# Performance work log

Measured on AMD Instinct MI355X. Metric: run time of the kernel, lower is better.

Reference implementation:

```python
import jax, jax.numpy as jnp
import numpy as np

NUM_EXPERTS = 256
TOP_K = 8
HIDDEN = 7168
N_GROUP = 8
TOPK_GROUP = 4
ROUTED_SCALING_FACTOR = 2.5
NORM_TOPK_PROB = True
TOKENS = 8192


def setup_inputs() -> dict:
    key = jax.random.key(0)
    k1, k2, k3 = jax.random.split(key, 3)
    hidden_states = jax.random.normal(k1, (TOKENS, HIDDEN), dtype=jnp.float32)
    # small init scale keeps router logits in a reasonable sigmoid range
    weight = jax.random.normal(k2, (NUM_EXPERTS, HIDDEN), dtype=jnp.float32) * 0.02
    e_score_correction_bias = jax.random.normal(k3, (NUM_EXPERTS,), dtype=jnp.float32) * 0.01
    return {
        "hidden_states": hidden_states,
        "weight": weight,
        "e_score_correction_bias": e_score_correction_bias,
    }


def reference(hidden_states, weight, e_score_correction_bias):
    hs = hidden_states.reshape(-1, hidden_states.shape[-1]).astype(jnp.float32)
    # [T, E] router logits -> sigmoid scores
    router_logits = hs @ weight.astype(jnp.float32).T
    scores = jax.nn.sigmoid(router_logits)
    scores_for_choice = scores + e_score_correction_bias[None, :]

    experts_per_group = NUM_EXPERTS // N_GROUP
    T = scores_for_choice.shape[0]
    # group score = sum of top-2 biased scores within each group  [T, G]
    grouped = scores_for_choice.reshape(T, N_GROUP, experts_per_group)
    top2_vals, _ = jax.lax.top_k(grouped, 2)
    group_scores = top2_vals.sum(axis=-1)

    # select top groups and build group mask  [T, G]
    _, group_idx = jax.lax.top_k(group_scores, TOPK_GROUP)
    group_mask = jnp.zeros_like(group_scores).at[
        jnp.arange(T)[:, None], group_idx
    ].set(1.0)

    # expand group mask to experts and zero out non-selected groups  [T, E]
    score_mask = jnp.broadcast_to(
        group_mask[:, :, None], (T, N_GROUP, experts_per_group)
    ).reshape(T, NUM_EXPERTS)
    masked_scores = jnp.where(score_mask.astype(bool), scores_for_choice, 0.0)

    # top-k experts over masked biased scores, weights gathered from raw scores
    _, topk_indices = jax.lax.top_k(masked_scores, TOP_K)
    topk_weights = jnp.take_along_axis(scores, topk_indices, axis=1)
    if NORM_TOPK_PROB:
        topk_weights = topk_weights / (
            topk_weights.sum(axis=-1, keepdims=True) + 1e-20
        )
    topk_weights = topk_weights * ROUTED_SCALING_FACTOR
    return topk_indices, topk_weights
```

## Files before the change

### kernel.cpp

```cpp
#include <hip/hip_runtime.h>
#include <float.h>
#include <math.h>

#define TOKENS 8192
#define EXPERTS 256
#define HIDDEN 7168
#define TOPK 8
#define TOPKG 4

#define BM 64
#define BN 256
#define BK 32
#define KSPLIT 8
#define KQ (HIDDEN / KSPLIT)
#define NKTB (KQ / BK)

#define TAU_E 6.0e-6f
#define TAU_G 1.2e-5f
#define MAXFB 1024

#define WIMG_ELEMS 1835008

typedef __attribute__((ext_vector_type(8))) short bf16x8;
typedef __attribute__((ext_vector_type(16))) float f32x16;

__device__ inline ushort bf16_rne(float x) {
    uint u = __float_as_uint(x);
    return (ushort)((u + 0x7FFFu + ((u >> 16) & 1u)) >> 16);
}
__device__ inline float bf16_tof(ushort h) { return __uint_as_float((uint)h << 16); }

#define CVTPK(lo, hi) ({ uint r_; asm("v_cvt_pk_bf16_f32 %0, %1, %2" : "=v"(r_) : "v"(lo), "v"(hi)); r_; })
__device__ inline float lo16f(uint u) { return __uint_as_float(u << 16); }
__device__ inline float hi16f(uint u) { return __uint_as_float(u & 0xFFFF0000u); }

#define BAR() do {                                             \
    asm volatile("s_waitcnt lgkmcnt(0)" ::: "memory");         \
    __builtin_amdgcn_s_barrier();                              \
    __builtin_amdgcn_sched_barrier(0);                         \
} while (0)

__global__ __launch_bounds__(256) void split_w(const float* __restrict__ W,
                                               ushort* __restrict__ wh,
                                               ushort* __restrict__ wl,
                                               int* __restrict__ cnt) {
    if (blockIdx.x == 0 && threadIdx.x == 0) *cnt = 0;
    const int tau  = blockIdx.x * 256 + threadIdx.x;
    const int j    = tau & 7;
    const int lane = (tau >> 3) & 63;
    const int cg   = (tau >> 9) & 7;
    const int kt16 = tau >> 12;
    const int col  = cg * 32 + (lane & 31);
    const int k    = kt16 * 16 + (lane >> 5) * 8 + j;
    const float w  = W[(size_t)col * HIDDEN + k];
    const ushort h = bf16_rne(w);
    const ushort l = bf16_rne(w - bf16_tof(h));
    wh[tau] = h;
    wl[tau] = l;
}

template <bool ATOMIC>
__global__ __launch_bounds__(512, 4) void logits_mfma(const float* __restrict__ A,
                                                      const ushort* __restrict__ wh,
                                                      const ushort* __restrict__ wl,
                                                      float* __restrict__ dst) {
    __shared__ ushort Ah[2][BM * BK];
    __shared__ ushort Al[2][BM * BK];

    const int b  = blockIdx.x;
    const int ks = b & 7;
    const int mb = b >> 3;
    const int row0 = mb * BM;

    const int t = threadIdx.x, lane = t & 63, wn = t >> 6;

    const int sr = t >> 3, q = t & 7;
    const float* Ap = A + (size_t)(row0 + sr) * HIDDEN + (size_t)ks * KQ + q * 4;
    const int sswz = ((sr >> 1) ^ (sr >> 3)) & 3;
    const int sidx = sr * 32 + ((((q >> 1)) ^ sswz) << 3) + (q & 1) * 4;

    int fidx[2][2];
    #pragma unroll
    for (int mi = 0; mi < 2; ++mi) {
        const int r = mi * 32 + (lane & 31);
        const int swz = ((r >> 1) ^ (r >> 3)) & 3;
        #pragma unroll
        for (int kh = 0; kh < 2; ++kh)
            fidx[mi][kh] = r * 32 + (((kh * 2 + (lane >> 5)) ^ swz) << 3);
    }

    const int wlanes = lane * 8;

    f32x16 acc[2];
    acc[0] = (f32x16)0.f;
    acc[1] = (f32x16)0.f;

    float4 aA, aB;
    bf16x8 wAh[2], wAl[2], wBh[2], wBl[2];

    #define WLOAD(DH, DL, KTL) do {                                            \
        const size_t wo = ((size_t)((ks * NKTB + (KTL)) * 2) * 8 + wn) * 512 + wlanes; \
        DH[0] = *(const bf16x8*)(wh + wo);                                     \
        DH[1] = *(const bf16x8*)(wh + wo + 4096);                              \
        DL[0] = *(const bf16x8*)(wl + wo);                                     \
        DL[1] = *(const bf16x8*)(wl + wo + 4096);                              \
    } while (0)

    #define STAGE(BB, R) do {                                                  \
        uint h0 = CVTPK(R.x, R.y), h1 = CVTPK(R.z, R.w);                       \
        float q0 = R.x - lo16f(h0), q1 = R.y - hi16f(h0);                      \
        float q2 = R.z - lo16f(h1), q3 = R.w - hi16f(h1);                      \
        uint l0 = CVTPK(q0, q1), l1 = CVTPK(q2, q3);                           \
        *(uint2*)&Ah[BB][sidx] = make_uint2(h0, h1);                           \
        *(uint2*)&Al[BB][sidx] = make_uint2(l0, l1);                           \
    } while (0)

    #define ALOAD(R, KTL) do {                                                 \
        const int ka = ((KTL) < NKTB ? (KTL) : NKTB - 1) * BK;                 \
        R = *(const float4*)(Ap + ka);                                         \
    } while (0)

    #define MF __builtin_amdgcn_mfma_f32_32x32x16_bf16

    #define ITER(KT, BB, X, WXH, WXL, WYH, WYL) do {                           \
        BAR();                                                                 \
        bf16x8 afh[2][2], afl[2][2];                                           \
        afh[0][0] = *(const bf16x8*)&Ah[BB][fidx[0][0]];                       \
        afh[0][1] = *(const bf16x8*)&Ah[BB][fidx[0][1]];                       \
        afh[1][0] = *(const bf16x8*)&Ah[BB][fidx[1][0]];                       \
        afh[1][1] = *(const bf16x8*)&Ah[BB][fidx[1][1]];                       \
        afl[0][0] = *(const bf16x8*)&Al[BB][fidx[0][0]];                       \
        afl[0][1] = *(const bf16x8*)&Al[BB][fidx[0][1]];                       \
        afl[1][0] = *(const bf16x8*)&Al[BB][fidx[1][0]];                       \
        afl[1][1] = *(const bf16x8*)&Al[BB][fidx[1][1]];                       \
        STAGE((BB) ^ 1, X);                                                    \
        ALOAD(X, (KT) + 3);                                                    \
        WLOAD(WYH, WYL, ((KT) + 1 < NKTB ? (KT) + 1 : NKTB - 1));              \
        acc[0] = MF(afh[0][0], WXH[0], acc[0], 0, 0, 0);                       \
        acc[0] = MF(afl[0][0], WXH[0], acc[0], 0, 0, 0);                       \
        acc[0] = MF(afh[0][0], WXL[0], acc[0], 0, 0, 0);                       \
        acc[1] = MF(afh[1][0], WXH[0], acc[1], 0, 0, 0);                       \
        acc[1] = MF(afl[1][0], WXH[0], acc[1], 0, 0, 0);                       \
        acc[1] = MF(afh[1][0], WXL[0], acc[1], 0, 0, 0);                       \
        acc[0] = MF(afh[0][1], WXH[1], acc[0], 0, 0, 0);                       \
        acc[0] = MF(afl[0][1], WXH[1], acc[0], 0, 0, 0);                       \
        acc[0] = MF(afh[0][1], WXL[1], acc[0], 0, 0, 0);                       \
        acc[1] = MF(afh[1][1], WXH[1], acc[1], 0, 0, 0);                       \
        acc[1] = MF(afl[1][1], WXH[1], acc[1], 0, 0, 0);                       \
        acc[1] = MF(afh[1][1], WXL[1], acc[1], 0, 0, 0);                       \
    } while (0)

    ALOAD(aA, 0);
    STAGE(0, aA);
    ALOAD(aA, 1);
    ALOAD(aB, 2);
    WLOAD(wAh, wAl, 0);

    for (int kt2 = 0; kt2 < NKTB; kt2 += 2) {
        ITER(kt2,     0, aA, wAh, wAl, wBh, wBl);
        ITER(kt2 + 1, 1, aB, wBh, wBl, wAh, wAl);
    }

    float* o = ATOMIC ? dst : dst + (size_t)ks * TOKENS * EXPERTS;
    #pragma unroll
    for (int mi = 0; mi < 2; ++mi)
        #pragma unroll
        for (int g = 0; g < 16; ++g) {
            const int row = row0 + mi * 32 + (g & 3) + ((g >> 2) << 3) + ((lane >> 5) << 2);
            const int col = wn * 32 + (lane & 31);
            const size_t idx = (size_t)row * EXPERTS + col;
            if (ATOMIC) atomicAdd(o + idx, acc[mi][g]);
            else        o[idx] = acc[mi][g];
        }
    #undef ITER
    #undef MF
    #undef ALOAD
    #undef STAGE
    #undef WLOAD
}

template <int NPART>
__global__ __launch_bounds__(256) void route_margin(const float* __restrict__ p0,
                                                    const float* __restrict__ bias,
                                                    float* __restrict__ out,
                                                    int* __restrict__ cnt,
                                                    int* __restrict__ list) {
    const int lane = threadIdx.x & 63;
    const int t    = blockIdx.x * 4 + (threadIdx.x >> 6);

    float4 lg = *(const float4*)(p0 + (size_t)t * EXPERTS + (lane << 2));
    #pragma unroll
    for (int p = 1; p < NPART; ++p) {
        const float4 l2 = *(const float4*)(p0 + (size_t)p * TOKENS * EXPERTS +
                                           (size_t)t * EXPERTS + (lane << 2));
        lg.x += l2.x; lg.y += l2.y; lg.z += l2.z; lg.w += l2.w;
    }
    const float4 bz = *(const float4*)(bias + (lane << 2));

    const float s0 = 1.f / (1.f + expf(-lg.x));
    const float s1 = 1.f / (1.f + expf(-lg.y));
    const float s2 = 1.f / (1.f + expf(-lg.z));
    const float s3 = 1.f / (1.f + expf(-lg.w));
    const float b0 = s0 + bz.x, b1 = s1 + bz.y, b2 = s2 + bz.z, b3 = s3 + bz.w;

    float hi01 = fmaxf(b0, b1), lo01 = fminf(b0, b1);
    float hi23 = fmaxf(b2, b3), lo23 = fminf(b2, b3);
    float a0v = fmaxf(hi01, hi23);
    float a1v = fmaxf(fminf(hi01, hi23), fmaxf(lo01, lo23));
    #pragma unroll
    for (int off = 1; off < 8; off <<= 1) {
        float o0 = __shfl_xor(a0v, off);
        float o1 = __shfl_xor(a1v, off);
        float n0 = fmaxf(a0v, o0);
        float n1 = fmaxf(fminf(a0v, o0), fmaxf(a1v, o1));
        a0v = n0; a1v = n1;
    }
    const float gscore = a0v + a1v;

    float gsc[8];
    #pragma unroll
    for (int g = 0; g < 8; ++g) gsc[g] = __shfl(gscore, g << 3);

    const int g0 = lane >> 3;
    int myrank = 0;
    float v4 = -1e30f, v5 = -1e30f;
    #pragma unroll
    for (int h = 0; h < 8; ++h) {
        int rk = 0;
        #pragma unroll
        for (int h2 = 0; h2 < 8; ++h2)
            rk += ((gsc[h2] > gsc[h]) || (gsc[h2] == gsc[h] && h2 < h)) ? 1 : 0;
        if (h == g0) myrank = rk;
        if (rk == TOPKG - 1) v4 = gsc[h];
        if (rk == TOPKG)     v5 = gsc[h];
    }
    const bool sel = (myrank < TOPKG);
    const float margin_g = v4 - v5;

    float m0 = sel ? b0 : 0.f;
    float m1 = sel ? b1 : 0.f;
    float m2 = sel ? b2 : 0.f;
    float m3 = sel ? b3 : 0.f;

    float sum = 0.f;
    int myidx = 0; float mysc = 0.f;
    float prev = 0.f, mine = 1e30f;
    #pragma unroll
    for (int rr = 0; rr < TOPK + 1; ++rr) {
        float bv = m0; int bj = 0;
        if (m1 > bv) { bv = m1; bj = 1; }
        if (m2 > bv) { bv = m2; bj = 2; }
        if (m3 > bv) { bv = m3; bj = 3; }
        float bsc = (bj == 0) ? s0 : (bj == 1) ? s1 : (bj == 2) ? s2 : s3;
        int bidx = (lane << 2) | bj;
        #pragma unroll
        for (int off = 1; off < 64; off <<= 1) {
            float ov  = __shfl_xor(bv, off);
            int   oi  = __shfl_xor(bidx, off);
            float osc = __shfl_xor(bsc, off);
            if (ov > bv || (ov == bv && oi < bidx)) { bv = ov; bidx = oi; bsc = osc; }
        }
        if (rr) mine = fminf(mine, prev - bv);
        prev = bv;
        if (rr < TOPK) {
            sum += bsc;
            if (lane == rr) { myidx = bidx; mysc = bsc; }
            if ((bidx >> 2) == lane) {
                const int sl = bidx & 3;
                if      (sl == 0) m0 = -FLT_MAX;
                else if (sl == 1) m1 = -FLT_MAX;
                else if (sl == 2) m2 = -FLT_MAX;
                else              m3 = -FLT_MAX;
            }
        }
    }

    const bool fb = (margin_g < TAU_G) || (mine < TAU_E);
    if (fb) {
        if (lane == 0) { int p = atomicAdd(cnt, 1); if (p < MAXFB) list[p] = t; }
    } else if (lane < TOPK) {
        const size_t base = (size_t)t * TOPK + lane;
        out[base] = (float)myidx;
        out[(size_t)TOKENS * TOPK + base] = mysc / (sum + 1e-20f) * 2.5f;
    }
}

__global__ __launch_bounds__(256) void fallback_logits(const float* __restrict__ A,
                                                       const float* __restrict__ W,
                                                       const int* __restrict__ cnt,
                                                       const int* __restrict__ list,
                                                       double* __restrict__ lgs) {
    const int n = min(*cnt, MAXFB);
    if (n == 0) return;
    __shared__ float Wsh[HIDDEN];
    const int e = blockIdx.x;
    const int tid = threadIdx.x;

    const float4* wg = (const float4*)(W + (size_t)e * HIDDEN);
    for (int i = tid; i < HIDDEN / 4; i += 256)
        ((float4*)Wsh)[i] = wg[i];
    __syncthreads();

    const int lane = tid & 63, wv = tid >> 6;
    for (int ti = wv; ti < n; ti += 4) {
        const int t = list[ti];
        const float* ar = A + (size_t)t * HIDDEN;
        double ac = 0.0;
        #pragma unroll 4
        for (int it = 0; it < HIDDEN / 256; ++it) {
            const int k = it * 256 + (lane << 2);
            const float4 a4 = *(const float4*)(ar + k);
            const float4 w4 = *(const float4*)&Wsh[k];
            ac = fma((double)a4.x, (double)w4.x, ac);
            ac = fma((double)a4.y, (double)w4.y, ac);
            ac = fma((double)a4.z, (double)w4.z, ac);
            ac = fma((double)a4.w, (double)w4.w, ac);
        }
        #pragma unroll
        for (int off = 32; off; off >>= 1)
            ac += __shfl_xor(ac, off);
        if (lane == 0)
            lgs[(size_t)ti * EXPERTS + e] = ac;
    }
}

__global__ __launch_bounds__(256) void fallback_route(const double* __restrict__ lgs,
                                                      const float* __restrict__ bias,
                                                      const int* __restrict__ cnt,
                                                      const int* __restrict__ list,
                                                      float* __restrict__ out) {
    const int n  = min(*cnt, MAXFB);
    const int ti = blockIdx.x * 4 + (threadIdx.x >> 6);
    if (ti >= n) return;
    const int lane = threadIdx.x & 63;
    const int t = list[ti];

    const double l0 = lgs[(size_t)ti * EXPERTS + (lane << 2)];
    const double l1 = lgs[(size_t)ti * EXPERTS + (lane << 2) + 1];
    const double l2 = lgs[(size_t)ti * EXPERTS + (lane << 2) + 2];
    const double l3 = lgs[(size_t)ti * EXPERTS + (lane << 2) + 3];
    const float4 bzf = *(const float4*)(bias + (lane << 2));

    const double s0 = 1.0 / (1.0 + exp(-l0));
    const double s1 = 1.0 / (1.0 + exp(-l1));
    const double s2 = 1.0 / (1.0 + exp(-l2));
    const double s3 = 1.0 / (1.0 + exp(-l3));
    const double b0 = s0 + (double)bzf.x, b1 = s1 + (double)bzf.y;
    const double b2 = s2 + (double)bzf.z, b3 = s3 + (double)bzf.w;

    double hi01 = fmax(b0, b1), lo01 = fmin(b0, b1);
    double hi23 = fmax(b2, b3), lo23 = fmin(b2, b3);
    double a0v = fmax(hi01, hi23);
    double a1v = fmax(fmin(hi01, hi23), fmax(lo01, lo23));
    #pragma unroll
    for (int off = 1; off < 8; off <<= 1) {
        double o0 = __shfl_xor(a0v, off);
        double o1 = __shfl_xor(a1v, off);
        double n0 = fmax(a0v, o0);
        double n1 = fmax(fmin(a0v, o0), fmax(a1v, o1));
        a0v = n0; a1v = n1;
    }
    const double gscore = a0v + a1v;
    double gsc[8];
    #pragma unroll
    for (int g = 0; g < 8; ++g) gsc[g] = __shfl(gscore, g << 3);
    const int g0 = lane >> 3;
    int rank = 0;
    #pragma unroll
    for (int h = 0; h < 8; ++h)
        rank += ((gsc[h] > gscore) || (gsc[h] == gscore && h < g0)) ? 1 : 0;
    const bool sel = (rank < TOPKG);

    double m0 = sel ? b0 : 0.0;
    double m1 = sel ? b1 : 0.0;
    double m2 = sel ? b2 : 0.0;
    double m3 = sel ? b3 : 0.0;

    double sum = 0.0;
    int myidx = 0; double mysc = 0.0;
    #pragma unroll
    for (int rr = 0; rr < TOPK; ++rr) {
        double bv = m0; int bj = 0;
        if (m1 > bv) { bv = m1; bj = 1; }
        if (m2 > bv) { bv = m2; bj = 2; }
        if (m3 > bv) { bv = m3; bj = 3; }
        double bsc = (bj == 0) ? s0 : (bj == 1) ? s1 : (bj == 2) ? s2 : s3;
        int bidx = (lane << 2) | bj;
        #pragma unroll
        for (int off = 1; off < 64; off <<= 1) {
            double ov  = __shfl_xor(bv, off);
            int    oi  = __shfl_xor(bidx, off);
            double osc = __shfl_xor(bsc, off);
            if (ov > bv || (ov == bv && oi < bidx)) { bv = ov; bidx = oi; bsc = osc; }
        }
        sum += bsc;
        if (lane == rr) { myidx = bidx; mysc = bsc; }
        if ((bidx >> 2) == lane) {
            const int sl = bidx & 3;
            if      (sl == 0) m0 = -DBL_MAX;
            else if (sl == 1) m1 = -DBL_MAX;
            else if (sl == 2) m2 = -DBL_MAX;
            else              m3 = -DBL_MAX;
        }
    }
    if (lane < TOPK) {
        const size_t base = (size_t)t * TOPK + lane;
        out[base] = (float)myidx;
        out[(size_t)TOKENS * TOPK + base] = (float)(mysc / (sum + 1e-20) * 2.5);
    }
}

extern "C" void kernel_launch(void* const* d_in, const int* in_sizes, int n_in,
                              void* d_out, int out_size, void* d_ws, size_t ws_size,
                              hipStream_t stream) {
    const float* hs   = (const float*)d_in[0];
    const float* wt   = (const float*)d_in[1];
    const float* bias = (const float*)d_in[2];
    float* out = (float*)d_out;
    char* ws = (char*)d_ws;

    const size_t LGSZ = (size_t)TOKENS * EXPERTS * 4;
    const size_t WIMG = (size_t)WIMG_ELEMS * 2;
    const int NBLK = (TOKENS / BM) * KSPLIT;

    if (ws_size >= KSPLIT * LGSZ + 131072 + 2 * WIMG) {
        float*  part  = (float*)ws;
        int*    cnt   = (int*)(ws + KSPLIT * LGSZ);
        int*    list  = (int*)(ws + KSPLIT * LGSZ + 256);
        ushort* wsh   = (ushort*)(ws + KSPLIT * LGSZ + 131072);
        ushort* wsl   = (ushort*)(ws + KSPLIT * LGSZ + 131072 + WIMG);
        double* lgs64 = (double*)ws;

        split_w<<<WIMG_ELEMS / 256, 256, 0, stream>>>(wt, wsh, wsl, cnt);
        logits_mfma<false><<<NBLK, 512, 0, stream>>>(hs, wsh, wsl, part);
        route_margin<KSPLIT><<<TOKENS / 4, 256, 0, stream>>>(part, bias, out, cnt, list);
        fallback_logits<<<EXPERTS, 256, 0, stream>>>(hs, wt, cnt, list, lgs64);
        fallback_route<<<MAXFB / 4, 256, 0, stream>>>(lgs64, bias, cnt, list, out);
    } else {
        float*  logits = (float*)ws;
        int*    cnt    = (int*)(ws + LGSZ);
        int*    list   = (int*)(ws + LGSZ + 256);
        ushort* wsh    = (ushort*)(ws + LGSZ + 131072);
        ushort* wsl    = (ushort*)(ws + LGSZ + 131072 + WIMG);
        double* lgs64  = (double*)ws;

        hipMemsetAsync(logits, 0, LGSZ, stream);
        split_w<<<WIMG_ELEMS / 256, 256, 0, stream>>>(wt, wsh, wsl, cnt);
        logits_mfma<true><<<NBLK, 512, 0, stream>>>(hs, wsh, wsl, logits);
        route_margin<1><<<TOKENS / 4, 256, 0, stream>>>(logits, bias, out, cnt, list);
        fallback_logits<<<EXPERTS, 256, 0, stream>>>(hs, wt, cnt, list, lgs64);
        fallback_route<<<MAXFB / 4, 256, 0, stream>>>(lgs64, bias, cnt, list, out);
    }
}
```

Before: 201.1 us.

## Split LDS fragment loads into halves interleaved with MFMA and raise wave priority

Each K iteration of the router GEMM now reads the LDS fragments for the first 32-row sub-tile, stages the next A tile and then synchronises. It then issues the acc[0] MFMAs at raised wave priority before reading the second sub-tile's fragments and running the acc[1] MFMAs. The scheduling barrier after each workgroup barrier is removed, so the compiler can reorder around it. A barrier is added after the prologue to fit the new sync placement. The aim is to overlap LDS reads and global loads with matrix-core work. The cost is a second workgroup barrier per iteration and less control over instruction order.

```diff
diff --git a/kernel.cpp b/kernel.cpp
--- a/kernel.cpp
+++ b/kernel.cpp
@@ -37,7 +37,6 @@
 #define BAR() do {                                             \
     asm volatile("s_waitcnt lgkmcnt(0)" ::: "memory");         \
     __builtin_amdgcn_s_barrier();                              \
-    __builtin_amdgcn_sched_barrier(0);                         \
 } while (0)
 
 __global__ __launch_bounds__(256) void split_w(const float* __restrict__ W,
@@ -123,31 +122,37 @@
     #define MF __builtin_amdgcn_mfma_f32_32x32x16_bf16
 
     #define ITER(KT, BB, X, WXH, WXL, WYH, WYL) do {                           \
+                                                        \
+        bf16x8 afh0a = *(const bf16x8*)&Ah[BB][fidx[0][0]];                    \
+        bf16x8 afh0b = *(const bf16x8*)&Ah[BB][fidx[0][1]];                    \
+        bf16x8 afl0a = *(const bf16x8*)&Al[BB][fidx[0][0]];                    \
+        bf16x8 afl0b = *(const bf16x8*)&Al[BB][fidx[0][1]];                    \
+        STAGE((BB) ^ 1, X);                                                    \
         BAR();                                                                 \
-        bf16x8 afh[2][2], afl[2][2];                                           \
-        afh[0][0] = *(const bf16x8*)&Ah[BB][fidx[0][0]];                       \
-        afh[0][1] = *(const bf16x8*)&Ah[BB][fidx[0][1]];                       \
-        afh[1][0] = *(const bf16x8*)&Ah[BB][fidx[1][0]];                       \
-        afh[1][1] = *(const bf16x8*)&Ah[BB][fidx[1][1]];                       \
-        afl[0][0] = *(const bf16x8*)&Al[BB][fidx[0][0]];                       \
-        afl[0][1] = *(const bf16x8*)&Al[BB][fidx[0][1]];                       \
-        afl[1][0] = *(const bf16x8*)&Al[BB][fidx[1][0]];                       \
-        afl[1][1] = *(const bf16x8*)&Al[BB][fidx[1][1]];                       \
-        STAGE((BB) ^ 1, X);                                                    \
+        __builtin_amdgcn_s_setprio(1);                                         \
+        acc[0] = MF(afh0a, WXH[0], acc[0], 0, 0, 0);                           \
+        acc[0] = MF(afl0a, WXH[0], acc[0], 0, 0, 0);                           \
+        acc[0] = MF(afh0a, WXL[0], acc[0], 0, 0, 0);                           \
+        acc[0] = MF(afh0b, WXH[1], acc[0], 0, 0, 0);                           \
+        acc[0] = MF(afl0b, WXH[1], acc[0], 0, 0, 0);                           \
+        acc[0] = MF(afh0b, WXL[1], acc[0], 0, 0, 0);                           \
+        __builtin_amdgcn_s_setprio(0);                                         \
+                                                        \
+        bf16x8 afh1a = *(const bf16x8*)&Ah[BB][fidx[1][0]];                    \
+        bf16x8 afh1b = *(const bf16x8*)&Ah[BB][fidx[1][1]];                    \
+        bf16x8 afl1a = *(const bf16x8*)&Al[BB][fidx[1][0]];                    \
+        bf16x8 afl1b = *(const bf16x8*)&Al[BB][fidx[1][1]];                    \
         ALOAD(X, (KT) + 3);                                                    \
         WLOAD(WYH, WYL, ((KT) + 1 < NKTB ? (KT) + 1 : NKTB - 1));              \
-        acc[0] = MF(afh[0][0], WXH[0], acc[0], 0, 0, 0);                       \
-        acc[0] = MF(afl[0][0], WXH[0], acc[0], 0, 0, 0);                       \
-        acc[0] = MF(afh[0][0], WXL[0], acc[0], 0, 0, 0);                       \
-        acc[1] = MF(afh[1][0], WXH[0], acc[1], 0, 0, 0);                       \
-        acc[1] = MF(afl[1][0], WXH[0], acc[1], 0, 0, 0);                       \
-        acc[1] = MF(afh[1][0], WXL[0], acc[1], 0, 0, 0);                       \
-        acc[0] = MF(afh[0][1], WXH[1], acc[0], 0, 0, 0);                       \
-        acc[0] = MF(afl[0][1], WXH[1], acc[0], 0, 0, 0);                       \
-        acc[0] = MF(afh[0][1], WXL[1], acc[0], 0, 0, 0);                       \
-        acc[1] = MF(afh[1][1], WXH[1], acc[1], 0, 0, 0);                       \
-        acc[1] = MF(afl[1][1], WXH[1], acc[1], 0, 0, 0);                       \
-        acc[1] = MF(afh[1][1], WXL[1], acc[1], 0, 0, 0);                       \
+        BAR();                                                                 \
+        __builtin_amdgcn_s_setprio(1);                                         \
+        acc[1] = MF(afh1a, WXH[0], acc[1], 0, 0, 0);                           \
+        acc[1] = MF(afl1a, WXH[0], acc[1], 0, 0, 0);                           \
+        acc[1] = MF(afh1a, WXL[0], acc[1], 0, 0, 0);                           \
+        acc[1] = MF(afh1b, WXH[1], acc[1], 0, 0, 0);                           \
+        acc[1] = MF(afl1b, WXH[1], acc[1], 0, 0, 0);                           \
+        acc[1] = MF(afh1b, WXL[1], acc[1], 0, 0, 0);                           \
+        __builtin_amdgcn_s_setprio(0);                                         \
     } while (0)
 
     ALOAD(aA, 0);
@@ -155,6 +160,7 @@
     ALOAD(aA, 1);
     ALOAD(aB, 2);
     WLOAD(wAh, wAl, 0);
+    BAR();
 
     for (int kt2 = 0; kt2 < NKTB; kt2 += 2) {
         ITER(kt2,     0, aA, wAh, wAl, wBh, wBl);
```

Result: faster. 193.3 us, median of 2 (-3.9%).

## Stage whole split-K A slice in LDS upfront and double K-split count

Applied to the files above, without the earlier changes.

The logits GEMM now loads, converts and stores the block's entire A slice (64 rows by the K-split chunk, as hi/lo bf16) into LDS before the MFMA loop. This removes the per-iteration double-buffer barriers and A staging from the inner loop. The K split is doubled to 16 so the slice fits in LDS. The cost is large LDS use, which forces one block per CU. The global A load is no longer overlapped with compute, and there are twice as many partial sums to reduce or atomically add.

```diff
diff --git a/kernel.cpp b/kernel.cpp
--- a/kernel.cpp
+++ b/kernel.cpp
@@ -11,7 +11,7 @@
 #define BM 64
 #define BN 256
 #define BK 32
-#define KSPLIT 8
+#define KSPLIT 16
 #define KQ (HIDDEN / KSPLIT)
 #define NKTB (KQ / BK)
 
@@ -33,12 +33,6 @@
 #define CVTPK(lo, hi) ({ uint r_; asm("v_cvt_pk_bf16_f32 %0, %1, %2" : "=v"(r_) : "v"(lo), "v"(hi)); r_; })
 __device__ inline float lo16f(uint u) { return __uint_as_float(u << 16); }
 __device__ inline float hi16f(uint u) { return __uint_as_float(u & 0xFFFF0000u); }
-
-#define BAR() do {                                             \
-    asm volatile("s_waitcnt lgkmcnt(0)" ::: "memory");         \
-    __builtin_amdgcn_s_barrier();                              \
-    __builtin_amdgcn_sched_barrier(0);                         \
-} while (0)
 
 __global__ __launch_bounds__(256) void split_w(const float* __restrict__ W,
                                                ushort* __restrict__ wh,
@@ -60,34 +54,49 @@
 }
 
 template <bool ATOMIC>
-__global__ __launch_bounds__(512, 4) void logits_mfma(const float* __restrict__ A,
+__global__ __launch_bounds__(512, 1) void logits_mfma(const float* __restrict__ A,
                                                       const ushort* __restrict__ wh,
                                                       const ushort* __restrict__ wl,
                                                       float* __restrict__ dst) {
-    __shared__ ushort Ah[2][BM * BK];
-    __shared__ ushort Al[2][BM * BK];
+    __shared__ ushort Ah[BM * KQ];
+    __shared__ ushort Al[BM * KQ];
 
     const int b  = blockIdx.x;
-    const int ks = b & 7;
-    const int mb = b >> 3;
+    const int ks = b & 15;
+    const int mb = b >> 4;
     const int row0 = mb * BM;
 
     const int t = threadIdx.x, lane = t & 63, wn = t >> 6;
 
-    const int sr = t >> 3, q = t & 7;
-    const float* Ap = A + (size_t)(row0 + sr) * HIDDEN + (size_t)ks * KQ + q * 4;
-    const int sswz = ((sr >> 1) ^ (sr >> 3)) & 3;
-    const int sidx = sr * 32 + ((((q >> 1)) ^ sswz) << 3) + (q & 1) * 4;
-
-    int fidx[2][2];
+    {
+        const int srow = t >> 3;
+        const int sk4  = (t & 7) << 2;
+        const float* Ap = A + (size_t)(row0 + srow) * HIDDEN + (size_t)ks * KQ;
+        const int sw = ((srow >> 1) ^ (srow >> 3)) & 3;
+        #pragma unroll
+        for (int c = 0; c < NKTB; ++c) {
+            const int k = c * 32 + sk4;
+            const float4 v = *(const float4*)(Ap + k);
+            const uint h0 = CVTPK(v.x, v.y), h1 = CVTPK(v.z, v.w);
+            const float q0 = v.x - lo16f(h0), q1 = v.y - hi16f(h0);
+            const float q2 = v.z - lo16f(h1), q3 = v.w - hi16f(h1);
+            const uint l0 = CVTPK(q0, q1), l1 = CVTPK(q2, q3);
+            const int idx = srow * KQ + (((k >> 3) ^ sw) << 3) + (k & 7);
+            *(uint2*)&Ah[idx] = make_uint2(h0, h1);
+            *(uint2*)&Al[idx] = make_uint2(l0, l1);
+        }
+    }
+    __syncthreads();
+
+    int fbase[2];
+    int fswz[2];
     #pragma unroll
     for (int mi = 0; mi < 2; ++mi) {
         const int r = mi * 32 + (lane & 31);
-        const int swz = ((r >> 1) ^ (r >> 3)) & 3;
-        #pragma unroll
-        for (int kh = 0; kh < 2; ++kh)
-            fidx[mi][kh] = r * 32 + (((kh * 2 + (lane >> 5)) ^ swz) << 3);
-    }
+        fbase[mi] = r * KQ;
+        fswz[mi]  = ((r >> 1) ^ (r >> 3)) & 3;
+    }
+    const int lsel = lane >> 5;
 
     const int wlanes = lane * 8;
 
@@ -95,7 +104,6 @@
     acc[0] = (f32x16)0.f;
     acc[1] = (f32x16)0.f;
 
-    float4 aA, aB;
     bf16x8 wAh[2], wAl[2], wBh[2], wBl[2];
 
     #define WLOAD(DH, DL, KTL) do {                                            \
@@ -106,36 +114,18 @@
         DL[1] = *(const bf16x8*)(wl + wo + 4096);                              \
     } while (0)
 
-    #define STAGE(BB, R) do {                                                  \
-        uint h0 = CVTPK(R.x, R.y), h1 = CVTPK(R.z, R.w);                       \
-        float q0 = R.x - lo16f(h0), q1 = R.y - hi16f(h0);                      \
-        float q2 = R.z - lo16f(h1), q3 = R.w - hi16f(h1);                      \
-        uint l0 = CVTPK(q0, q1), l1 = CVTPK(q2, q3);                           \
-        *(uint2*)&Ah[BB][sidx] = make_uint2(h0, h1);                           \
-        *(uint2*)&Al[BB][sidx] = make_uint2(l0, l1);                           \
-    } while (0)
-
-    #define ALOAD(R, KTL) do {                                                 \
-        const int ka = ((KTL) < NKTB ? (KTL) : NKTB - 1) * BK;                 \
-        R = *(const float4*)(Ap + ka);                                         \
-    } while (0)
-
     #define MF __builtin_amdgcn_mfma_f32_32x32x16_bf16
 
-    #define ITER(KT, BB, X, WXH, WXL, WYH, WYL) do {                           \
-        BAR();                                                                 \
+    #define ITER(KT, WXH, WXL, WYH, WYL) do {                                  \
+        WLOAD(WYH, WYL, ((KT) + 1 < NKTB ? (KT) + 1 : NKTB - 1));              \
         bf16x8 afh[2][2], afl[2][2];                                           \
-        afh[0][0] = *(const bf16x8*)&Ah[BB][fidx[0][0]];                       \
-        afh[0][1] = *(const bf16x8*)&Ah[BB][fidx[0][1]];                       \
-        afh[1][0] = *(const bf16x8*)&Ah[BB][fidx[1][0]];                       \
-        afh[1][1] = *(const bf16x8*)&Ah[BB][fidx[1][1]];                       \
-        afl[0][0] = *(const bf16x8*)&Al[BB][fidx[0][0]];                       \
-        afl[0][1] = *(const bf16x8*)&Al[BB][fidx[0][1]];                       \
-        afl[1][0] = *(const bf16x8*)&Al[BB][fidx[1][0]];                       \
-        afl[1][1] = *(const bf16x8*)&Al[BB][fidx[1][1]];                       \
-        STAGE((BB) ^ 1, X);                                                    \
-        ALOAD(X, (KT) + 3);                                                    \
-        WLOAD(WYH, WYL, ((KT) + 1 < NKTB ? (KT) + 1 : NKTB - 1));              \
+        _Pragma("unroll") for (int mi = 0; mi < 2; ++mi)                       \
+            _Pragma("unroll") for (int kh = 0; kh < 2; ++kh) {                 \
+                const int oct = (KT) * 4 + kh * 2 + lsel;                      \
+                const int idx = fbase[mi] + ((oct ^ fswz[mi]) << 3);           \
+                afh[mi][kh] = *(const bf16x8*)&Ah[idx];                        \
+                afl[mi][kh] = *(const bf16x8*)&Al[idx];                        \
+            }                                                                  \
         acc[0] = MF(afh[0][0], WXH[0], acc[0], 0, 0, 0);                       \
         acc[0] = MF(afl[0][0], WXH[0], acc[0], 0, 0, 0);                       \
         acc[0] = MF(afh[0][0], WXL[0], acc[0], 0, 0, 0);                       \
@@ -150,15 +140,11 @@
         acc[1] = MF(afh[1][1], WXL[1], acc[1], 0, 0, 0);                       \
     } while (0)
 
-    ALOAD(aA, 0);
-    STAGE(0, aA);
-    ALOAD(aA, 1);
-    ALOAD(aB, 2);
     WLOAD(wAh, wAl, 0);
-
+    #pragma unroll
     for (int kt2 = 0; kt2 < NKTB; kt2 += 2) {
-        ITER(kt2,     0, aA, wAh, wAl, wBh, wBl);
-        ITER(kt2 + 1, 1, aB, wBh, wBl, wAh, wAl);
+        ITER(kt2,     wAh, wAl, wBh, wBl);
+        ITER(kt2 + 1, wBh, wBl, wAh, wAl);
     }
 
     float* o = ATOMIC ? dst : dst + (size_t)ks * TOKENS * EXPERTS;
@@ -174,8 +160,6 @@
         }
     #undef ITER
     #undef MF
-    #undef ALOAD
-    #undef STAGE
     #undef WLOAD
 }
 
```

Result: slower. 268.9 us (+33.7%).
